# Performance work log

Measured on AMD Instinct MI355X. Metric: run time of the kernel, lower is better.

The kernel has to match this reference:

```python
import jax, jax.numpy as jnp
import numpy as np
import math

C = 512
NUM_HEADS = 4
GROUPS = 32  # group_count(512, 32)
EPS = 1e-5


def group_norm(x, gamma, beta):
    # x: [b, c, h, w]; normalize over (c//GROUPS, h, w) per group
    b, c, h, w = x.shape
    xg = x.reshape(b, GROUPS, -1)
    mu = jnp.mean(xg, axis=-1, keepdims=True)
    var = jnp.var(xg, axis=-1, keepdims=True)
    xn = ((xg - mu) * jax.lax.rsqrt(var + EPS)).reshape(b, c, h, w)
    return xn * gamma[None, :, None, None] + beta[None, :, None, None]


def setup_inputs() -> dict:
    key = jax.random.key(0)
    ks = jax.random.split(key, 5)
    b, h, w = 2, 64, 64
    x = jax.random.normal(ks[0], (b, C, h, w), dtype=jnp.float32)
    gn_w = jnp.ones((C,), dtype=jnp.float32)
    gn_b = jnp.zeros((C,), dtype=jnp.float32)
    s_qkv = 1.0 / math.sqrt(C)
    w_qkv = jax.random.uniform(ks[1], (3 * C, C), jnp.float32, -s_qkv, s_qkv)
    b_qkv = jax.random.uniform(ks[2], (3 * C,), jnp.float32, -s_qkv, s_qkv)
    w_proj = jax.random.uniform(ks[3], (C, C), jnp.float32, -s_qkv, s_qkv)
    b_proj = jax.random.uniform(ks[4], (C,), jnp.float32, -s_qkv, s_qkv)
    return {"x": x, "gn_w": gn_w, "gn_b": gn_b, "w_qkv": w_qkv,
            "b_qkv": b_qkv, "w_proj": w_proj, "b_proj": b_proj}


def reference(x, gn_w, gn_b, w_qkv, b_qkv, w_proj, b_proj):
    b, c, h, w = x.shape
    L = h * w
    nh = NUM_HEADS
    hd = c // nh
    residual = x
    xn = group_norm(x, gn_w, gn_b).reshape(b, c, L)
    # Conv1d with kernel_size=1 == channelwise linear: [b, 3c, L]
    qkv = jnp.einsum('bcl,oc->bol', xn, w_qkv) + b_qkv[None, :, None]
    q, k, v = jnp.split(qkv, 3, axis=1)
    q = q.reshape(b, nh, hd, L)
    k = k.reshape(b, nh, hd, L)
    v = v.reshape(b, nh, hd, L)
    scores = jnp.einsum('bncd,bnce->bnde', q, k) / math.sqrt(hd)
    attn = jax.nn.softmax(scores, axis=-1)
    out = jnp.einsum('bnde,bnce->bncd', attn, v).reshape(b, c, L)
    out = jnp.einsum('bcl,oc->bol', out, w_proj) + b_proj[None, :, None]
    return out.reshape(b, c, h, w) + residual
```

## Files before the change

### kernel.cpp

```cpp
#include <hip/hip_runtime.h>
#include <math.h>

typedef __bf16 bf16;
typedef __bf16 bf16x8 __attribute__((ext_vector_type(8)));
typedef __bf16 bf16x4 __attribute__((ext_vector_type(4)));
typedef float f32x4 __attribute__((ext_vector_type(4)));

#define QSCALE (0.08838834764831845f * 1.4426950408889634f)

__device__ __forceinline__ void gll16(const bf16* g, bf16* l) {
    __builtin_amdgcn_global_load_lds((const __attribute__((address_space(1))) void*)g,
                                     (__attribute__((address_space(3))) void*)l, 16, 0, 0);
}

__global__ void k_pre(const float* __restrict__ wqkv, const float* __restrict__ wproj,
                      const float* __restrict__ x,
                      bf16* __restrict__ wqkv_b, bf16* __restrict__ wproj_b,
                      float* __restrict__ part) {
    int blk = blockIdx.x;
    if (blk < 1024) {
        int i = blk * 256 + threadIdx.x;
        const int n1 = (1536 * 512) / 4;
        float4 v;
        bf16* dst;
        if (i < n1) { v = ((const float4*)wqkv)[i];      dst = wqkv_b + (size_t)i * 4; }
        else        { v = ((const float4*)wproj)[i - n1]; dst = wproj_b + (size_t)(i - n1) * 4; }
        bf16x4 o;
        o[0] = (bf16)v.x; o[1] = (bf16)v.y; o[2] = (bf16)v.z; o[3] = (bf16)v.w;
        *(bf16x4*)dst = o;
        return;
    }
    int b2 = blk - 1024;
    int grp = b2 >> 2, p = b2 & 3;
    const float4* src = (const float4*)(x + (size_t)grp * 65536 + (size_t)p * 16384);
    float s = 0.f, ss = 0.f;
    for (int it = 0; it < 16; ++it) {
        float4 v = src[threadIdx.x + it * 256];
        s  += v.x + v.y + v.z + v.w;
        ss += v.x * v.x + v.y * v.y + v.z * v.z + v.w * v.w;
    }
    for (int off = 32; off; off >>= 1) { s += __shfl_down(s, off); ss += __shfl_down(ss, off); }
    __shared__ float rs[4], rss[4];
    int wave = threadIdx.x >> 6;
    if ((threadIdx.x & 63) == 0) { rs[wave] = s; rss[wave] = ss; }
    __syncthreads();
    if (threadIdx.x == 0) {
        part[(grp * 4 + p) * 2]     = rs[0] + rs[1] + rs[2] + rs[3];
        part[(grp * 4 + p) * 2 + 1] = rss[0] + rss[1] + rss[2] + rss[3];
    }
}

__global__ __launch_bounds__(256) void k_gn_norm_t(const float* __restrict__ x, const float* __restrict__ gw,
                                                   const float* __restrict__ gb, const float* __restrict__ part,
                                                   bf16* __restrict__ xn_t) {
    __shared__ float sX[64 * 69];
    __shared__ float sMean[4], sRstd[4];
    int b = blockIdx.z, c0 = blockIdx.y * 64, l0 = blockIdx.x * 64;
    int t = threadIdx.x;
    if (t < 4) {
        int g = b * 32 + (c0 >> 4) + t;
        float S = 0.f, SS = 0.f;
        for (int p = 0; p < 4; ++p) { S += part[(g * 4 + p) * 2]; SS += part[(g * 4 + p) * 2 + 1]; }
        float mean = S * (1.f / 65536.f);
        float var  = SS * (1.f / 65536.f) - mean * mean;
        sMean[t] = mean;
        sRstd[t] = rsqrtf(var + 1e-5f);
    }
    __syncthreads();
    int cr = t >> 4, lq = t & 15;
    const float* xp = x + ((size_t)(b * 512 + c0)) * 4096 + l0;
    for (int i = 0; i < 4; ++i) {
        int c = cr + i * 16;
        int cg = c0 + c;
        float mean = sMean[c >> 4], rstd = sRstd[c >> 4];
        float ga = gw[cg] * rstd;
        float be = gb[cg] - mean * ga;
        float4 v = *(const float4*)(xp + (size_t)c * 4096 + lq * 4);
        float* d = &sX[c * 69 + lq * 4];
        d[0] = v.x * ga + be; d[1] = v.y * ga + be; d[2] = v.z * ga + be; d[3] = v.w * ga + be;
    }
    __syncthreads();
    int lr = t >> 3, cp = t & 7;
    bf16* dst = xn_t + ((size_t)b * 4096 + l0) * 512 + c0;
    for (int i = 0; i < 2; ++i) {
        int l = lr + i * 32;
        bf16x8 o;
        for (int j = 0; j < 8; ++j) o[j] = (bf16)sX[(cp * 8 + j) * 69 + l];
        *(bf16x8*)(dst + (size_t)l * 512 + cp * 8) = o;
    }
}

__global__ __launch_bounds__(256, 3) void k_gemm_qkv(
    const bf16* __restrict__ A, const bf16* __restrict__ W, const float* __restrict__ bias,
    bf16* __restrict__ qkT, bf16* __restrict__ vb) {
    __shared__ bf16 smem[17408];
    int linear = blockIdx.x + 12 * blockIdx.y + 384 * blockIdx.z;
    int swz = (linear & 7) * 96 + (linear >> 3);
    int n0 = (swz % 12) * 128;
    int m0 = ((swz / 12) % 32) * 128;
    int bz = swz / 384;
    int tid = threadIdx.x, lane = tid & 63, wave = tid >> 6;
    int lo = lane & 15, quad = lane >> 4;
    int lr = lane >> 3, ls = lane & 7;
    int mw = (wave >> 1) * 64, nw = (wave & 1) * 64;
    const bf16* aptr[4]; int adst[4];
    const bf16* bptr[4]; int bdst[4];
    for (int i = 0; i < 4; ++i) {
        int r0 = wave * 32 + i * 8;
        int row = r0 + lr;
        aptr[i] = A + (size_t)bz * (4096 * 512) + (size_t)(m0 + row) * 512 + ((ls ^ (row & 7)) * 8);
        adst[i] = r0 * 64;
        bptr[i] = W + (size_t)(n0 + row) * 512 + ((ls ^ (row & 7)) * 8);
        bdst[i] = 8192 + r0 * 64;
    }
    f32x4 acc[4][4] = {};
    for (int step = 0; step < 8; ++step) {
        __syncthreads();
        for (int i = 0; i < 4; ++i) {
            gll16(aptr[i], &smem[adst[i]]); aptr[i] += 64;
            gll16(bptr[i], &smem[bdst[i]]); bptr[i] += 64;
        }
        __syncthreads();
        const bf16* sA = smem;
        const bf16* sB = smem + 8192;
        for (int kk = 0; kk < 2; ++kk) {
            bf16x8 af[4], bfr[4];
            int sw = ((kk * 4 + quad) ^ (lo & 7)) * 8;
            for (int t = 0; t < 4; ++t) af[t]  = *(const bf16x8*)&sA[(mw + t * 16 + lo) * 64 + sw];
            for (int t = 0; t < 4; ++t) bfr[t] = *(const bf16x8*)&sB[(nw + t * 16 + lo) * 64 + sw];
            for (int mt = 0; mt < 4; ++mt)
                for (int nt = 0; nt < 4; ++nt)
                    acc[mt][nt] = __builtin_amdgcn_mfma_f32_16x16x32_bf16(af[mt], bfr[nt], acc[mt][nt], 0, 0, 0);
        }
    }
    __syncthreads();
    bf16* sT = smem;
    bool isv = (n0 >= 1024);
    float sc = (n0 < 512) ? QSCALE : 1.f;
    for (int mt = 0; mt < 4; ++mt)
        for (int nt = 0; nt < 4; ++nt) {
            int c = nw + nt * 16 + lo;
            float bv = bias[n0 + c];
            for (int r = 0; r < 4; ++r) {
                int l = mw + mt * 16 + quad * 4 + r;
                float v = (acc[mt][nt][r] + bv) * sc;
                if (isv) sT[c * 136 + l] = (bf16)v;
                else     sT[l * 136 + c] = (bf16)v;
            }
        }
    __syncthreads();
    int row = tid >> 1, hh = tid & 1;
    if (isv) {
        bf16* dst = vb + (size_t)bz * (512 * 4096) + (size_t)(n0 - 1024 + row) * 4096 + m0;
        for (int j = 0; j < 8; ++j) {
            int ch = hh + j * 2;
            *(bf16x8*)(dst + ch * 8) = *(const bf16x8*)&sT[row * 136 + ch * 8];
        }
    } else {
        bf16* dst = qkT + (size_t)bz * (4096 * 1024) + (size_t)(m0 + row) * 1024 + n0;
        for (int j = 0; j < 8; ++j) {
            int ch = hh + j * 2;
            *(bf16x8*)(dst + ch * 8) = *(const bf16x8*)&sT[row * 136 + ch * 8];
        }
    }
}

__global__ __launch_bounds__(256, 3) void k_gemm_proj(
    const bf16* __restrict__ W, const bf16* __restrict__ Bm,
    const float* __restrict__ bias_m,
    float* __restrict__ outf, const float* __restrict__ resid) {
    constexpr int BUF = (64 + 128) * 64;
    __shared__ bf16 smem[2 * BUF];
    int bz = blockIdx.z;
    int m0 = blockIdx.y * 64, n0 = blockIdx.x * 128;
    int tid = threadIdx.x, lane = tid & 63, wave = tid >> 6;
    int lo = lane & 15, quad = lane >> 4;
    int lr = lane >> 3, ls = lane & 7;
    int mw = (wave >> 1) * 32, nw = (wave & 1) * 64;
    const bf16* aptr[2]; int adst[2];
    for (int i = 0; i < 2; ++i) {
        int r0 = wave * 16 + i * 8;
        int row = r0 + lr;
        aptr[i] = W + (size_t)(m0 + row) * 512 + ((ls ^ (row & 7)) * 8);
        adst[i] = r0 * 64;
    }
    const bf16* bptr[4]; int bdst[4];
    for (int i = 0; i < 4; ++i) {
        int r0 = wave * 32 + i * 8;
        int row = r0 + lr;
        bptr[i] = Bm + (size_t)bz * (4096 * 512) + (size_t)(n0 + row) * 512 + ((ls ^ (row & 7)) * 8);
        bdst[i] = 64 * 64 + r0 * 64;
    }
    f32x4 acc[2][4] = {};
    for (int i = 0; i < 2; ++i) { gll16(aptr[i], &smem[adst[i]]); aptr[i] += 64; }
    for (int i = 0; i < 4; ++i) { gll16(bptr[i], &smem[bdst[i]]); bptr[i] += 64; }
    for (int step = 0; step < 8; ++step) {
        int cur = step & 1;
        __syncthreads();
        if (step < 7) {
            bf16* nb = &smem[(cur ^ 1) * BUF];
            for (int i = 0; i < 2; ++i) { gll16(aptr[i], nb + adst[i]); aptr[i] += 64; }
            for (int i = 0; i < 4; ++i) { gll16(bptr[i], nb + bdst[i]); bptr[i] += 64; }
        }
        const bf16* sA = &smem[cur * BUF];
        const bf16* sB = sA + 64 * 64;
        for (int kk = 0; kk < 2; ++kk) {
            bf16x8 af[2], bfr[4];
            int sw = ((kk * 4 + quad) ^ (lo & 7)) * 8;
            for (int t = 0; t < 2; ++t) af[t]  = *(const bf16x8*)&sA[(mw + t * 16 + lo) * 64 + sw];
            for (int t = 0; t < 4; ++t) bfr[t] = *(const bf16x8*)&sB[(nw + t * 16 + lo) * 64 + sw];
            for (int mt = 0; mt < 2; ++mt)
                for (int nt = 0; nt < 4; ++nt)
                    acc[mt][nt] = __builtin_amdgcn_mfma_f32_16x16x32_bf16(af[mt], bfr[nt], acc[mt][nt], 0, 0, 0);
        }
    }
    for (int mt = 0; mt < 2; ++mt) {
        int rowb = m0 + mw + mt * 16 + quad * 4;
        for (int nt = 0; nt < 4; ++nt) {
            int col = n0 + nw + nt * 16 + lo;
            for (int r = 0; r < 4; ++r) {
                int row = rowb + r;
                size_t idx = (size_t)bz * (512 * 4096) + (size_t)row * 4096 + col;
                outf[idx] = acc[mt][nt][r] + bias_m[row] + resid[idx];
            }
        }
    }
}

__global__ __launch_bounds__(512, 2) void k_attn(const bf16* __restrict__ qkT, const bf16* __restrict__ vmat,
                                                 bf16* __restrict__ attnT) {
    __shared__ __align__(16) char smem[163840];
    bf16* sE = (bf16*)smem;
    int bidx = blockIdx.x;
    int bh = bidx & 7;
    int bb = bh >> 2, h = bh & 3;
    int l0 = (bidx >> 3) * 128;
    int tid = threadIdx.x, lane = tid & 63, wave = tid >> 6;
    int lo = lane & 15, quad = lane >> 4;
    int a = wave & 3, b2 = wave >> 2;
    const bf16* qbase = qkT + ((size_t)bb * 4096 + l0) * 1024 + h * 128;
    const bf16* kbase = qkT + (size_t)bb * 4096 * 1024 + 512 + h * 128;
    const bf16* vbase = vmat + (size_t)(bb * 512 + h * 128) * 4096;
    for (int i = 0; i < 4; ++i) {
        int r0 = wave * 16 + i * 4;
        int row = r0 + quad;
        gll16(qbase + (size_t)row * 1024 + ((lo ^ (row & 15)) * 8), sE + r0 * 128);
    }
    __syncthreads();
    bf16x8 qf[2][4];
    for (int nt = 0; nt < 2; ++nt) {
        int row = a * 32 + nt * 16 + lo;
        for (int kk = 0; kk < 4; ++kk)
            qf[nt][kk] = *(const bf16x8*)&sE[row * 128 + (((kk * 4 + quad) ^ lo) * 8)];
    }
    __syncthreads();
    const bf16* kp[4]; int kdst[4];
    const bf16* vp[4]; int vdst[4];
    for (int i = 0; i < 4; ++i) {
        int r0 = wave * 16 + i * 4;
        int row = r0 + quad;
        kp[i] = kbase + (size_t)row * 1024 + ((lo ^ (row & 15)) * 8);
        kdst[i] = r0 * 128;
        vp[i] = vbase + (size_t)row * 4096 + ((lo ^ (row & 15)) * 8);
        vdst[i] = 32768 + r0 * 128;
    }
    char* sPb = smem + 131072 + wave * 4096;
    int swz8 = lo & 7;
    float l_r[2];
    l_r[0] = l_r[1] = 0.f;
    f32x4 oacc[8][2] = {};
    for (int i = 0; i < 4; ++i) { gll16(kp[i], sE + kdst[i]); kp[i] += (size_t)128 * 1024; }
    for (int i = 0; i < 4; ++i) { gll16(vp[i], sE + vdst[i]); vp[i] += 128; }
    for (int it = 0; it < 32; ++it) {
        int cur = it & 1;
        __syncthreads();
        if (it < 31) {
            int nb = (cur ^ 1) * 16384;
            for (int i = 0; i < 4; ++i) { gll16(kp[i], sE + nb + kdst[i]); kp[i] += (size_t)128 * 1024; }
            for (int i = 0; i < 4; ++i) { gll16(vp[i], sE + nb + vdst[i]); vp[i] += 128; }
        }
        const bf16* sK = sE + cur * 16384;
        const bf16* sV = sE + 32768 + cur * 16384;
        for (int mt = 0; mt < 4; ++mt) {
            int krow = b2 * 64 + mt * 16 + lo;
            f32x4 s0 = {}, s1 = {};
            __builtin_amdgcn_s_setprio(1);
            for (int kk = 0; kk < 4; ++kk) {
                bf16x8 kf = *(const bf16x8*)&sK[krow * 128 + (((kk * 4 + quad) ^ lo) * 8)];
                s0 = __builtin_amdgcn_mfma_f32_16x16x32_bf16(kf, qf[0][kk], s0, 0, 0, 0);
                s1 = __builtin_amdgcn_mfma_f32_16x16x32_bf16(kf, qf[1][kk], s1, 0, 0, 0);
            }
            __builtin_amdgcn_s_setprio(0);
            int cw = (((2 * mt + (quad >> 1)) ^ swz8) << 4) + ((quad & 1) << 3);
            float sm0 = 0.f, sm1 = 0.f;
            bf16x4 pk;
            for (int r = 0; r < 4; ++r) { float pv = __builtin_amdgcn_exp2f(s0[r]); sm0 += pv; pk[r] = (bf16)pv; }
            *(bf16x4*)&sPb[lo * 128 + cw] = pk;
            for (int r = 0; r < 4; ++r) { float pv = __builtin_amdgcn_exp2f(s1[r]); sm1 += pv; pk[r] = (bf16)pv; }
            *(bf16x4*)&sPb[(16 + lo) * 128 + cw] = pk;
            l_r[0] += sm0;
            l_r[1] += sm1;
        }
        bf16x8 pf[2][2];
        for (int nt = 0; nt < 2; ++nt)
            for (int kk = 0; kk < 2; ++kk)
                pf[nt][kk] = *(const bf16x8*)&sPb[(nt * 16 + lo) * 128 + (((kk * 4 + quad) ^ swz8) << 4)];
        __builtin_amdgcn_s_setprio(1);
        for (int mt2 = 0; mt2 < 8; ++mt2) {
            int vrow = mt2 * 16 + lo;
            for (int kk = 0; kk < 2; ++kk) {
                bf16x8 vf = *(const bf16x8*)&sV[vrow * 128 + (((b2 * 8 + kk * 4 + quad) ^ lo) * 8)];
                oacc[mt2][0] = __builtin_amdgcn_mfma_f32_16x16x32_bf16(vf, pf[0][kk], oacc[mt2][0], 0, 0, 0);
                oacc[mt2][1] = __builtin_amdgcn_mfma_f32_16x16x32_bf16(vf, pf[1][kk], oacc[mt2][1], 0, 0, 0);
            }
        }
        __builtin_amdgcn_s_setprio(0);
    }
    for (int nt = 0; nt < 2; ++nt) {
        l_r[nt] += __shfl_xor(l_r[nt], 16);
        l_r[nt] += __shfl_xor(l_r[nt], 32);
    }
    __syncthreads();
    float* sStat = (float*)(smem + 139264);
    if (quad == 0) {
        for (int nt = 0; nt < 2; ++nt) {
            int qb = a * 32 + nt * 16 + lo;
            sStat[qb * 2 + b2] = l_r[nt];
        }
    }
    __syncthreads();
    float inv[2];
    for (int nt = 0; nt < 2; ++nt) {
        int qb = a * 32 + nt * 16 + lo;
        inv[nt] = 1.f / (sStat[qb * 2] + sStat[qb * 2 + 1]);
    }
    float* sOm = (float*)smem;
    bf16* sOut = (bf16*)(smem + 67584);
    if (b2 == 1) {
        for (int mt2 = 0; mt2 < 8; ++mt2)
            for (int nt = 0; nt < 2; ++nt)
                for (int r = 0; r < 4; ++r) {
                    int vc = mt2 * 16 + quad * 4 + r;
                    sOm[a * 4224 + vc * 33 + nt * 16 + lo] = oacc[mt2][nt][r];
                }
    }
    __syncthreads();
    if (b2 == 0) {
        for (int mt2 = 0; mt2 < 8; ++mt2)
            for (int nt = 0; nt < 2; ++nt)
                for (int r = 0; r < 4; ++r) {
                    int vc = mt2 * 16 + quad * 4 + r;
                    float v = (oacc[mt2][nt][r] + sOm[a * 4224 + vc * 33 + nt * 16 + lo]) * inv[nt];
                    sOut[(a * 32 + nt * 16 + lo) * 136 + vc] = (bf16)v;
                }
    }
    __syncthreads();
    bf16* dst = attnT + ((size_t)bb * 4096 + l0) * 512 + h * 128;
    for (int i = 0; i < 4; ++i) {
        int row = (tid >> 4) + i * 32;
        int chunk = tid & 15;
        bf16x8 v = *(const bf16x8*)&sOut[row * 136 + chunk * 8];
        *(bf16x8*)(dst + (size_t)row * 512 + chunk * 8) = v;
    }
}

extern "C" void kernel_launch(void* const* d_in, const int* in_sizes, int n_in,
                              void* d_out, int out_size, void* d_ws, size_t ws_size,
                              hipStream_t stream) {
    const float* x      = (const float*)d_in[0];
    const float* gn_w   = (const float*)d_in[1];
    const float* gn_b   = (const float*)d_in[2];
    const float* w_qkv  = (const float*)d_in[3];
    const float* b_qkv  = (const float*)d_in[4];
    const float* w_proj = (const float*)d_in[5];
    const float* b_proj = (const float*)d_in[6];
    float* out = (float*)d_out;
    char* ws = (char*)d_ws;
    bf16* wqkv_b  = (bf16*)(ws + 0);
    bf16* wproj_b = (bf16*)(ws + 1572864);
    bf16* xn_t    = (bf16*)(ws + 2097152);
    bf16* qkT     = (bf16*)(ws + 10485760);
    bf16* vb      = (bf16*)(ws + 27262976);
    bf16* attnT   = (bf16*)(ws + 35651584);
    float* part   = (float*)(ws + 44040192);

    k_pre<<<1280, 256, 0, stream>>>(w_qkv, w_proj, x, wqkv_b, wproj_b, part);
    k_gn_norm_t<<<dim3(64, 8, 2), 256, 0, stream>>>(x, gn_w, gn_b, part, xn_t);
    k_gemm_qkv<<<dim3(12, 32, 2), 256, 0, stream>>>(xn_t, wqkv_b, b_qkv, qkT, vb);
    k_attn<<<256, 512, 0, stream>>>(qkT, vb, attnT);
    k_gemm_proj<<<dim3(32, 8, 2), 256, 0, stream>>>(wproj_b, attnT, b_proj, out, x);
}
```

Before: 188.9 us.

## Enlarge proj GEMM tile to 128x128 with XCD-aware block swizzle; batch attention QK MFMAs

The projection GEMM moves from a 64x128 to a 128x128 tile per block. This halves the grid to 256 blocks and raises MFMA work per LDS load. A block-index swizzle groups neighbouring tiles onto the same XCD for L2 reuse, and the occupancy hint in launch_bounds is removed, so fewer waves may be resident. In the attention kernel, all QK^T MFMAs for a tile are issued together under high priority before the exp/pack phase, which costs more live registers.

```diff
diff --git a/kernel.cpp b/kernel.cpp
--- a/kernel.cpp
+++ b/kernel.cpp
@@ -165,56 +165,59 @@
     }
 }
 
-__global__ __launch_bounds__(256, 3) void k_gemm_proj(
+__global__ __launch_bounds__(256) void k_gemm_proj(
     const bf16* __restrict__ W, const bf16* __restrict__ Bm,
     const float* __restrict__ bias_m,
     float* __restrict__ outf, const float* __restrict__ resid) {
-    constexpr int BUF = (64 + 128) * 64;
+    constexpr int BUF = (128 + 128) * 64;
     __shared__ bf16 smem[2 * BUF];
-    int bz = blockIdx.z;
-    int m0 = blockIdx.y * 64, n0 = blockIdx.x * 128;
+    int linear = blockIdx.x + 32 * blockIdx.y + 128 * blockIdx.z;
+    int swz = (linear & 7) * 32 + (linear >> 3);
+    int n0 = (swz % 32) * 128;
+    int m0 = ((swz / 32) % 4) * 128;
+    int bz = swz / 128;
     int tid = threadIdx.x, lane = tid & 63, wave = tid >> 6;
     int lo = lane & 15, quad = lane >> 4;
     int lr = lane >> 3, ls = lane & 7;
-    int mw = (wave >> 1) * 32, nw = (wave & 1) * 64;
-    const bf16* aptr[2]; int adst[2];
-    for (int i = 0; i < 2; ++i) {
-        int r0 = wave * 16 + i * 8;
+    int mw = (wave >> 1) * 64, nw = (wave & 1) * 64;
+    const bf16* aptr[4]; int adst[4];
+    const bf16* bptr[4]; int bdst[4];
+    for (int i = 0; i < 4; ++i) {
+        int r0 = wave * 32 + i * 8;
         int row = r0 + lr;
         aptr[i] = W + (size_t)(m0 + row) * 512 + ((ls ^ (row & 7)) * 8);
         adst[i] = r0 * 64;
-    }
-    const bf16* bptr[4]; int bdst[4];
-    for (int i = 0; i < 4; ++i) {
-        int r0 = wave * 32 + i * 8;
-        int row = r0 + lr;
         bptr[i] = Bm + (size_t)bz * (4096 * 512) + (size_t)(n0 + row) * 512 + ((ls ^ (row & 7)) * 8);
-        bdst[i] = 64 * 64 + r0 * 64;
-    }
-    f32x4 acc[2][4] = {};
-    for (int i = 0; i < 2; ++i) { gll16(aptr[i], &smem[adst[i]]); aptr[i] += 64; }
-    for (int i = 0; i < 4; ++i) { gll16(bptr[i], &smem[bdst[i]]); bptr[i] += 64; }
+        bdst[i] = 8192 + r0 * 64;
+    }
+    f32x4 acc[4][4] = {};
+    for (int i = 0; i < 4; ++i) {
+        gll16(aptr[i], &smem[adst[i]]); aptr[i] += 64;
+        gll16(bptr[i], &smem[bdst[i]]); bptr[i] += 64;
+    }
     for (int step = 0; step < 8; ++step) {
         int cur = step & 1;
         __syncthreads();
         if (step < 7) {
             bf16* nb = &smem[(cur ^ 1) * BUF];
-            for (int i = 0; i < 2; ++i) { gll16(aptr[i], nb + adst[i]); aptr[i] += 64; }
-            for (int i = 0; i < 4; ++i) { gll16(bptr[i], nb + bdst[i]); bptr[i] += 64; }
+            for (int i = 0; i < 4; ++i) {
+                gll16(aptr[i], nb + adst[i]); aptr[i] += 64;
+                gll16(bptr[i], nb + bdst[i]); bptr[i] += 64;
+            }
         }
         const bf16* sA = &smem[cur * BUF];
-        const bf16* sB = sA + 64 * 64;
+        const bf16* sB = sA + 8192;
         for (int kk = 0; kk < 2; ++kk) {
-            bf16x8 af[2], bfr[4];
+            bf16x8 af[4], bfr[4];
             int sw = ((kk * 4 + quad) ^ (lo & 7)) * 8;
-            for (int t = 0; t < 2; ++t) af[t]  = *(const bf16x8*)&sA[(mw + t * 16 + lo) * 64 + sw];
+            for (int t = 0; t < 4; ++t) af[t]  = *(const bf16x8*)&sA[(mw + t * 16 + lo) * 64 + sw];
             for (int t = 0; t < 4; ++t) bfr[t] = *(const bf16x8*)&sB[(nw + t * 16 + lo) * 64 + sw];
-            for (int mt = 0; mt < 2; ++mt)
+            for (int mt = 0; mt < 4; ++mt)
                 for (int nt = 0; nt < 4; ++nt)
                     acc[mt][nt] = __builtin_amdgcn_mfma_f32_16x16x32_bf16(af[mt], bfr[nt], acc[mt][nt], 0, 0, 0);
         }
     }
-    for (int mt = 0; mt < 2; ++mt) {
+    for (int mt = 0; mt < 4; ++mt) {
         int rowb = m0 + mw + mt * 16 + quad * 4;
         for (int nt = 0; nt < 4; ++nt) {
             int col = n0 + nw + nt * 16 + lo;
@@ -281,22 +284,27 @@
         }
         const bf16* sK = sE + cur * 16384;
         const bf16* sV = sE + 32768 + cur * 16384;
+        f32x4 s[4][2];
+        __builtin_amdgcn_s_setprio(1);
         for (int mt = 0; mt < 4; ++mt) {
             int krow = b2 * 64 + mt * 16 + lo;
             f32x4 s0 = {}, s1 = {};
-            __builtin_amdgcn_s_setprio(1);
             for (int kk = 0; kk < 4; ++kk) {
                 bf16x8 kf = *(const bf16x8*)&sK[krow * 128 + (((kk * 4 + quad) ^ lo) * 8)];
                 s0 = __builtin_amdgcn_mfma_f32_16x16x32_bf16(kf, qf[0][kk], s0, 0, 0, 0);
                 s1 = __builtin_amdgcn_mfma_f32_16x16x32_bf16(kf, qf[1][kk], s1, 0, 0, 0);
             }
-            __builtin_amdgcn_s_setprio(0);
+            s[mt][0] = s0;
+            s[mt][1] = s1;
+        }
+        __builtin_amdgcn_s_setprio(0);
+        for (int mt = 0; mt < 4; ++mt) {
             int cw = (((2 * mt + (quad >> 1)) ^ swz8) << 4) + ((quad & 1) << 3);
             float sm0 = 0.f, sm1 = 0.f;
             bf16x4 pk;
-            for (int r = 0; r < 4; ++r) { float pv = __builtin_amdgcn_exp2f(s0[r]); sm0 += pv; pk[r] = (bf16)pv; }
+            for (int r = 0; r < 4; ++r) { float pv = __builtin_amdgcn_exp2f(s[mt][0][r]); sm0 += pv; pk[r] = (bf16)pv; }
             *(bf16x4*)&sPb[lo * 128 + cw] = pk;
-            for (int r = 0; r < 4; ++r) { float pv = __builtin_amdgcn_exp2f(s1[r]); sm1 += pv; pk[r] = (bf16)pv; }
+            for (int r = 0; r < 4; ++r) { float pv = __builtin_amdgcn_exp2f(s[mt][1][r]); sm1 += pv; pk[r] = (bf16)pv; }
             *(bf16x4*)&sPb[(16 + lo) * 128 + cw] = pk;
             l_r[0] += sm0;
             l_r[1] += sm1;
@@ -388,5 +396,5 @@
     k_gn_norm_t<<<dim3(64, 8, 2), 256, 0, stream>>>(x, gn_w, gn_b, part, xn_t);
     k_gemm_qkv<<<dim3(12, 32, 2), 256, 0, stream>>>(xn_t, wqkv_b, b_qkv, qkT, vb);
     k_attn<<<256, 512, 0, stream>>>(qkT, vb, attnT);
-    k_gemm_proj<<<dim3(32, 8, 2), 256, 0, stream>>>(wproj_b, attnT, b_proj, out, x);
-}
+    k_gemm_proj<<<dim3(32, 4, 2), 256, 0, stream>>>(wproj_b, attnT, b_proj, out, x);
+}
```

New measurement: 184.4 us, median of 2. 2.3% less time.
